# Performance work log

Hardware: AMD Instinct MI355X
Metric: run time of the kernel (lower is better)

Reference implementation:

```python
import jax, jax.numpy as jnp
import numpy as np

V, D = 100000, 300          # vocab, embedding dim
B, L, T, C, I = 64, 256, 1, 10, 6  # batch, positions, targets, context, info samples


def setup_inputs() -> dict:
    key = jax.random.key(0)
    ks = jax.random.split(key, 8)
    # indices start at 1 so padding_idx=0 (zero row, no grad in torch) never appears
    pos_u = jax.random.randint(ks[0], (B, L, T), 1, V)
    pos_v = jax.random.randint(ks[1], (B, L, C), 1, V)
    info_v = jax.random.randint(ks[2], (B, L, I), 1, V)
    initrange = 1.0 / D
    W_out = jax.random.uniform(ks[3], (V, D), minval=-initrange, maxval=initrange, dtype=jnp.float32)
    # torch inits W_in to 0; use a small random init so the baseline is non-degenerate
    W_in = jax.random.uniform(ks[4], (V, D), minval=-initrange, maxval=initrange, dtype=jnp.float32)
    W_out = W_out.at[0].set(0.0)
    W_in = W_in.at[0].set(0.0)
    context_mask = (jax.random.uniform(ks[5], (C,)) > 0.2).astype(jnp.float32)
    sig_mask = jnp.where(jax.random.uniform(ks[6], (I,)) > 0.5, 1.0, -1.0).astype(jnp.float32)
    score_mask = jax.random.uniform(ks[7], (I,), dtype=jnp.float32)
    return {"pos_u": pos_u, "pos_v": pos_v, "info_v": info_v,
            "W_in": W_in, "W_out": W_out,
            "context_mask": context_mask, "sig_mask": sig_mask, "score_mask": score_mask}


def reference(pos_u, pos_v, info_v, W_in, W_out, context_mask, sig_mask, score_mask):
    tgt_out = W_out[pos_u]    # [B,L,T,D]
    ctx_in = W_in[pos_v]      # [B,L,C,D]
    ctx_out = W_out[pos_v]    # [B,L,C,D]
    info_in = W_in[info_v]    # [B,L,I,D]
    # dropout disabled (p=0, eval-mode determinism)
    ctx_in = ctx_in * context_mask[None, None, :, None]
    # target-context scores: [B,L,T,C]
    score = jnp.einsum('bltd,blcd->bltc', tgt_out, ctx_in)
    score = jnp.clip(score, -10.0, 10.0)
    loss = -jnp.sum(jax.nn.log_sigmoid(score))
    # context-info scores: [B,L,C,I]
    info_score = jnp.einsum('blcd,blid->blci', ctx_out, info_in)
    info_score = jnp.clip(info_score, -10.0, 10.0)
    info_score = info_score * sig_mask          # sign flip for negative samples
    info_score = -jax.nn.log_sigmoid(info_score) * score_mask
    return loss + jnp.sum(info_score)
```

## Files before the change

### kernel.cpp

```cpp
#include <hip/hip_runtime.h>

#define D_ 300
#define C_ 10
#define I_ 6
#define NPOS 16384
#define PPB 4
#define NBLK (NPOS / PPB)
#define CHUNK 35

__device__ __forceinline__ float neg_log_sigmoid(float x) {
    return __logf(1.0f + __expf(-x));
}

__global__ __launch_bounds__(256, 4) void hg2vec_pos_kernel(
    const int* __restrict__ pos_u, const int* __restrict__ pos_v,
    const int* __restrict__ info_v,
    const float* __restrict__ W_in, const float* __restrict__ W_out,
    const float* __restrict__ context_mask, const float* __restrict__ sig_mask,
    const float* __restrict__ score_mask, float* __restrict__ partial)
{
    const int wave = threadIdx.x >> 6;
    const int lane = threadIdx.x & 63;
    const int p = blockIdx.x * PPB + wave;

    __shared__ float s_red[PPB][CHUNK][65];
    __shared__ float s_wsum[PPB];

    const int su = __builtin_amdgcn_readfirstlane(pos_u[p]);
    int scv[C_], siv[I_];
#pragma unroll
    for (int c = 0; c < C_; ++c) scv[c] = __builtin_amdgcn_readfirstlane(pos_v[p * C_ + c]);
#pragma unroll
    for (int i = 0; i < I_; ++i) siv[i] = __builtin_amdgcn_readfirstlane(info_v[p * I_ + i]);

    const int k4 = lane + 256;
    const float okf = (k4 < D_) ? 1.0f : 0.0f;
    const int k4c = (k4 < D_) ? k4 : lane;

    const float* ur = W_out + (size_t)su * D_;
    float u0 = ur[lane], u1 = ur[lane + 64], u2 = ur[lane + 128], u3 = ur[lane + 192];
    float u4 = ur[k4c] * okf;

    float ii0[I_], ii1[I_], ii2[I_], ii3[I_], ii4[I_];
#pragma unroll
    for (int i = 0; i < I_; ++i) {
        const float* r = W_in + (size_t)siv[i] * D_;
        ii0[i] = r[lane];       ii1[i] = r[lane + 64];
        ii2[i] = r[lane + 128]; ii3[i] = r[lane + 192];
        ii4[i] = r[k4c] * okf;
    }

    float acc = 0.0f;

#pragma unroll
    for (int chunk = 0; chunk < 2; ++chunk) {
        float part[CHUNK];
#pragma unroll
        for (int cc = 0; cc < 5; ++cc) {
            const int c = chunk * 5 + cc;
            const float* cir = W_in  + (size_t)scv[c] * D_;
            const float* cor = W_out + (size_t)scv[c] * D_;
            float a0 = cir[lane], a1 = cir[lane + 64], a2 = cir[lane + 128],
                  a3 = cir[lane + 192], a4 = cir[k4c];
            float b0 = cor[lane], b1 = cor[lane + 64], b2 = cor[lane + 128],
                  b3 = cor[lane + 192], b4 = cor[k4c];
            part[cc * 7] = u0 * a0 + u1 * a1 + u2 * a2 + u3 * a3 + u4 * a4;
#pragma unroll
            for (int i = 0; i < I_; ++i)
                part[cc * 7 + 1 + i] =
                    b0 * ii0[i] + b1 * ii1[i] + b2 * ii2[i] + b3 * ii3[i] + b4 * ii4[i];
        }

        __syncthreads();
#pragma unroll
        for (int d = 0; d < CHUNK; ++d) s_red[wave][d][lane] = part[d];
        __syncthreads();

        if (lane < CHUNK) {
            float s0 = 0, s1 = 0, s2 = 0, s3 = 0;
#pragma unroll
            for (int l = 0; l < 64; l += 4) {
                s0 += s_red[wave][lane][l + 0];
                s1 += s_red[wave][lane][l + 1];
                s2 += s_red[wave][lane][l + 2];
                s3 += s_red[wave][lane][l + 3];
            }
            float dot = (s0 + s1) + (s2 + s3);
            const int cc = lane / 7;
            const int t  = lane - cc * 7;
            const int c  = chunk * 5 + cc;
            float term;
            if (t == 0) {
                float x = dot * context_mask[c];
                x = fminf(fmaxf(x, -10.0f), 10.0f);
                term = neg_log_sigmoid(x);
            } else {
                const int i = t - 1;
                float x = fminf(fmaxf(dot, -10.0f), 10.0f) * sig_mask[i];
                term = neg_log_sigmoid(x) * score_mask[i];
            }
            acc += term;
        }
    }

#pragma unroll
    for (int off = 32; off; off >>= 1) acc += __shfl_xor(acc, off, 64);
    if (lane == 0) s_wsum[wave] = acc;
    __syncthreads();
    if (threadIdx.x == 0)
        partial[blockIdx.x] = s_wsum[0] + s_wsum[1] + s_wsum[2] + s_wsum[3];
}

__global__ __launch_bounds__(1024) void hg2vec_reduce_kernel(
    const float* __restrict__ partial, float* __restrict__ out)
{
    float4 v = ((const float4*)partial)[threadIdx.x];
    float a = (v.x + v.y) + (v.z + v.w);
#pragma unroll
    for (int off = 32; off; off >>= 1) a += __shfl_xor(a, off, 64);
    __shared__ float s[16];
    if ((threadIdx.x & 63) == 0) s[threadIdx.x >> 6] = a;
    __syncthreads();
    if (threadIdx.x == 0) {
        float t = 0;
#pragma unroll
        for (int i = 0; i < 16; ++i) t += s[i];
        out[0] = t;
    }
}

extern "C" void kernel_launch(void* const* d_in, const int* in_sizes, int n_in,
                              void* d_out, int out_size, void* d_ws, size_t ws_size,
                              hipStream_t stream) {
    const int* pos_u = (const int*)d_in[0];
    const int* pos_v = (const int*)d_in[1];
    const int* info_v = (const int*)d_in[2];
    const float* W_in = (const float*)d_in[3];
    const float* W_out = (const float*)d_in[4];
    const float* context_mask = (const float*)d_in[5];
    const float* sig_mask = (const float*)d_in[6];
    const float* score_mask = (const float*)d_in[7];
    float* out = (float*)d_out;
    float* partial = (float*)d_ws;

    hg2vec_pos_kernel<<<NBLK, 256, 0, stream>>>(
        pos_u, pos_v, info_v, W_in, W_out,
        context_mask, sig_mask, score_mask, partial);
    hg2vec_reduce_kernel<<<1, 1024, 0, stream>>>(partial, out);
}
```

Before: 286.6 us.

## Pre-reduce dot products with lane shuffles to shrink LDS and raise occupancy

The per-lane partial dot products are first reduced across 8-lane groups with xor shuffles. Only one value per group goes to a much smaller shared buffer, and the 35-wide register staging array and block-wide syncthreads are removed. Launch bounds rise to 8 blocks per CU so more waves are in flight for this gather-bound kernel. Each wave now writes its own partial sum, and the final reduce kernel loops over 16384 partials with 256 threads. The change adds shuffle instructions and more partials to reduce, and it relies on intra-wave LDS ordering without an explicit barrier.

New measurement: 294.4 us. +2.7%, slower.

```diff
diff --git a/kernel.cpp b/kernel.cpp
--- a/kernel.cpp
+++ b/kernel.cpp
@@ -6,13 +6,14 @@
 #define NPOS 16384
 #define PPB 4
 #define NBLK (NPOS / PPB)
-#define CHUNK 35
+#define NDOT 70
+#define RED_LD 71
 
 __device__ __forceinline__ float neg_log_sigmoid(float x) {
     return __logf(1.0f + __expf(-x));
 }
 
-__global__ __launch_bounds__(256, 4) void hg2vec_pos_kernel(
+__global__ __launch_bounds__(256, 8) void hg2vec_pos_kernel(
     const int* __restrict__ pos_u, const int* __restrict__ pos_v,
     const int* __restrict__ info_v,
     const float* __restrict__ W_in, const float* __restrict__ W_out,
@@ -23,8 +24,7 @@
     const int lane = threadIdx.x & 63;
     const int p = blockIdx.x * PPB + wave;
 
-    __shared__ float s_red[PPB][CHUNK][65];
-    __shared__ float s_wsum[PPB];
+    __shared__ float s_red[PPB][8][RED_LD];
 
     const int su = __builtin_amdgcn_readfirstlane(pos_u[p]);
     int scv[C_], siv[I_];
@@ -38,8 +38,8 @@
     const int k4c = (k4 < D_) ? k4 : lane;
 
     const float* ur = W_out + (size_t)su * D_;
-    float u0 = ur[lane], u1 = ur[lane + 64], u2 = ur[lane + 128], u3 = ur[lane + 192];
-    float u4 = ur[k4c] * okf;
+    const float u0 = ur[lane], u1 = ur[lane + 64], u2 = ur[lane + 128],
+                u3 = ur[lane + 192], u4 = ur[k4c] * okf;
 
     float ii0[I_], ii1[I_], ii2[I_], ii3[I_], ii4[I_];
 #pragma unroll
@@ -50,83 +50,76 @@
         ii4[i] = r[k4c] * okf;
     }
 
-    float acc = 0.0f;
+    const int g = lane >> 3;
+    const bool writer = (lane & 7) == 0;
 
 #pragma unroll
-    for (int chunk = 0; chunk < 2; ++chunk) {
-        float part[CHUNK];
+    for (int c = 0; c < C_; ++c) {
+        const float* cir = W_in  + (size_t)scv[c] * D_;
+        const float* cor = W_out + (size_t)scv[c] * D_;
+        const float a0 = cir[lane], a1 = cir[lane + 64], a2 = cir[lane + 128],
+                    a3 = cir[lane + 192], a4 = cir[k4c];
+        const float b0 = cor[lane], b1 = cor[lane + 64], b2 = cor[lane + 128],
+                    b3 = cor[lane + 192], b4 = cor[k4c];
+
+        float part[7];
+        part[0] = u0 * a0 + u1 * a1 + u2 * a2 + u3 * a3 + u4 * a4;
 #pragma unroll
-        for (int cc = 0; cc < 5; ++cc) {
-            const int c = chunk * 5 + cc;
-            const float* cir = W_in  + (size_t)scv[c] * D_;
-            const float* cor = W_out + (size_t)scv[c] * D_;
-            float a0 = cir[lane], a1 = cir[lane + 64], a2 = cir[lane + 128],
-                  a3 = cir[lane + 192], a4 = cir[k4c];
-            float b0 = cor[lane], b1 = cor[lane + 64], b2 = cor[lane + 128],
-                  b3 = cor[lane + 192], b4 = cor[k4c];
-            part[cc * 7] = u0 * a0 + u1 * a1 + u2 * a2 + u3 * a3 + u4 * a4;
+        for (int i = 0; i < I_; ++i)
+            part[1 + i] = b0 * ii0[i] + b1 * ii1[i] + b2 * ii2[i] + b3 * ii3[i] + b4 * ii4[i];
+
 #pragma unroll
-            for (int i = 0; i < I_; ++i)
-                part[cc * 7 + 1 + i] =
-                    b0 * ii0[i] + b1 * ii1[i] + b2 * ii2[i] + b3 * ii3[i] + b4 * ii4[i];
+        for (int t = 0; t < 7; ++t) {
+            float v = part[t];
+            v += __shfl_xor(v, 1, 64);
+            v += __shfl_xor(v, 2, 64);
+            v += __shfl_xor(v, 4, 64);
+            if (writer) s_red[wave][g][c * 7 + t] = v;
         }
+    }
 
-        __syncthreads();
+    float acc = 0.0f;
 #pragma unroll
-        for (int d = 0; d < CHUNK; ++d) s_red[wave][d][lane] = part[d];
-        __syncthreads();
-
-        if (lane < CHUNK) {
-            float s0 = 0, s1 = 0, s2 = 0, s3 = 0;
-#pragma unroll
-            for (int l = 0; l < 64; l += 4) {
-                s0 += s_red[wave][lane][l + 0];
-                s1 += s_red[wave][lane][l + 1];
-                s2 += s_red[wave][lane][l + 2];
-                s3 += s_red[wave][lane][l + 3];
-            }
-            float dot = (s0 + s1) + (s2 + s3);
-            const int cc = lane / 7;
-            const int t  = lane - cc * 7;
-            const int c  = chunk * 5 + cc;
-            float term;
+    for (int pass = 0; pass < 2; ++pass) {
+        const int d = pass * 64 + lane;
+        if (d < NDOT) {
+            float s = s_red[wave][0][d] + s_red[wave][1][d] + s_red[wave][2][d]
+                    + s_red[wave][3][d] + s_red[wave][4][d] + s_red[wave][5][d]
+                    + s_red[wave][6][d] + s_red[wave][7][d];
+            const int c = d / 7;
+            const int t = d - c * 7;
             if (t == 0) {
-                float x = dot * context_mask[c];
+                float x = s * context_mask[c];
                 x = fminf(fmaxf(x, -10.0f), 10.0f);
-                term = neg_log_sigmoid(x);
+                acc += neg_log_sigmoid(x);
             } else {
                 const int i = t - 1;
-                float x = fminf(fmaxf(dot, -10.0f), 10.0f) * sig_mask[i];
-                term = neg_log_sigmoid(x) * score_mask[i];
+                float x = fminf(fmaxf(s, -10.0f), 10.0f) * sig_mask[i];
+                acc += neg_log_sigmoid(x) * score_mask[i];
             }
-            acc += term;
         }
     }
 
 #pragma unroll
     for (int off = 32; off; off >>= 1) acc += __shfl_xor(acc, off, 64);
-    if (lane == 0) s_wsum[wave] = acc;
-    __syncthreads();
-    if (threadIdx.x == 0)
-        partial[blockIdx.x] = s_wsum[0] + s_wsum[1] + s_wsum[2] + s_wsum[3];
+    if (lane == 0) partial[p] = acc;
 }
 
-__global__ __launch_bounds__(1024) void hg2vec_reduce_kernel(
+__global__ __launch_bounds__(256) void hg2vec_reduce_kernel(
     const float* __restrict__ partial, float* __restrict__ out)
 {
-    float4 v = ((const float4*)partial)[threadIdx.x];
-    float a = (v.x + v.y) + (v.z + v.w);
+    float a = 0.0f;
+    const float4* p4 = (const float4*)partial;
+    for (int i = threadIdx.x; i < NPOS / 4; i += 256) {
+        float4 v = p4[i];
+        a += (v.x + v.y) + (v.z + v.w);
+    }
 #pragma unroll
     for (int off = 32; off; off >>= 1) a += __shfl_xor(a, off, 64);
-    __shared__ float s[16];
+    __shared__ float s[4];
     if ((threadIdx.x & 63) == 0) s[threadIdx.x >> 6] = a;
     __syncthreads();
-    if (threadIdx.x == 0) {
-        float t = 0;
-#pragma unroll
-        for (int i = 0; i < 16; ++i) t += s[i];
-        out[0] = t;
-    }
+    if (threadIdx.x == 0) out[0] = (s[0] + s[1]) + (s[2] + s[3]);
 }
 
 extern "C" void kernel_launch(void* const* d_in, const int* in_sizes, int n_in,
@@ -146,5 +139,5 @@
     hg2vec_pos_kernel<<<NBLK, 256, 0, stream>>>(
         pos_u, pos_v, info_v, W_in, W_out,
         context_mask, sig_mask, score_mask, partial);
-    hg2vec_reduce_kernel<<<1, 1024, 0, stream>>>(partial, out);
+    hg2vec_reduce_kernel<<<1, 256, 0, stream>>>(partial, out);
 }
```
